# Performance work log

Measured on AMD Instinct MI355X. Metric: run time of the kernel, lower is better.

The kernel has to match this reference:

```python
import jax, jax.numpy as jnp
import numpy as np

N_HEADS = 16
N_KV_HEADS = 4
HEAD_DIM = 128


def _rope(x, cos, sin):
    # x: [b, s, h, d]; cos/sin: [s, d//2]; interleaved pair rotation
    b, s, h, d = x.shape
    xp = x.reshape(b, s, h, d // 2, 2)
    x_r, x_i = xp[..., 0], xp[..., 1]
    c = cos[None, :, None, :]
    sn = sin[None, :, None, :]
    o_r = x_r * c - x_i * sn
    o_i = x_r * sn + x_i * c
    return jnp.stack([o_r, o_i], axis=-1).reshape(b, s, h, d)


def setup_inputs() -> dict:
    key = jax.random.key(0)
    ks = jax.random.split(key, 7)
    B, S, D = 2, 2048, 2048
    KV = N_KV_HEADS * HEAD_DIM
    x = jax.random.normal(ks[0], (B, S, D), dtype=jnp.float32)
    freqs_cos = jax.random.uniform(ks[1], (S, HEAD_DIM // 2), dtype=jnp.float32)
    freqs_sin = jax.random.uniform(ks[2], (S, HEAD_DIM // 2), dtype=jnp.float32)
    scale = 0.02
    wq = jax.random.normal(ks[3], (D, D), dtype=jnp.float32) * scale
    wk = jax.random.normal(ks[4], (KV, D), dtype=jnp.float32) * scale
    wv = jax.random.normal(ks[5], (KV, D), dtype=jnp.float32) * scale
    wo = jax.random.normal(ks[6], (D, D), dtype=jnp.float32) * scale
    return {"x": x, "freqs_cos": freqs_cos, "freqs_sin": freqs_sin,
            "wq": wq, "wk": wk, "wv": wv, "wo": wo}


def reference(x, freqs_cos, freqs_sin, wq, wk, wv, wo):
    B, S, D = x.shape
    n_rep = N_HEADS // N_KV_HEADS
    q = (x @ wq.T).reshape(B, S, N_HEADS, HEAD_DIM)
    k = (x @ wk.T).reshape(B, S, N_KV_HEADS, HEAD_DIM)
    v = (x @ wv.T).reshape(B, S, N_KV_HEADS, HEAD_DIM)
    q = _rope(q, freqs_cos, freqs_sin)
    k = _rope(k, freqs_cos, freqs_sin)
    # repeat_kv == torch.repeat_interleave along head dim
    k = jnp.repeat(k, n_rep, axis=2)
    v = jnp.repeat(v, n_rep, axis=2)
    q = q.transpose(0, 2, 1, 3)  # [B, H, S, d]
    k = k.transpose(0, 2, 1, 3)
    v = v.transpose(0, 2, 1, 3)
    scale = 1.0 / np.sqrt(HEAD_DIM).astype(np.float32)
    scores = jnp.einsum('bhqd,bhkd->bhqk', q, k) * scale
    causal = jnp.tril(jnp.ones((S, S), dtype=bool))
    scores = jnp.where(causal[None, None], scores, jnp.finfo(jnp.float32).min)
    probs = jax.nn.softmax(scores.astype(jnp.float32), axis=-1).astype(q.dtype)
    out = jnp.einsum('bhqk,bhkd->bhqd', probs, v)
    out = out.transpose(0, 2, 1, 3).reshape(B, S, N_HEADS * HEAD_DIM)
    return out @ wo.T
```

## Files before the change

### kernel.cpp

```cpp
#include <hip/hip_runtime.h>
#include <hip/hip_bf16.h>
#include <type_traits>

using bf16x8 = __attribute__((ext_vector_type(8))) short;
using f32x4  = __attribute__((ext_vector_type(4))) float;
using u16x8  = __attribute__((ext_vector_type(8))) unsigned short;
using u16x4  = __attribute__((ext_vector_type(4))) unsigned short;
using u32x4  = __attribute__((ext_vector_type(4))) unsigned int;

__device__ __forceinline__ float b2f(unsigned short u) {
    unsigned int x = ((unsigned int)u) << 16;
    return __builtin_bit_cast(float, x);
}
__device__ __forceinline__ unsigned short f2b(float f) {
    __hip_bfloat16 h = __float2bfloat16(f);
    return __builtin_bit_cast(unsigned short, h);
}

#if defined(__has_builtin)
#if __has_builtin(__builtin_amdgcn_exp2f)
#define EXP2F(x) __builtin_amdgcn_exp2f(x)
#else
#define EXP2F(x) exp2f(x)
#endif
#else
#define EXP2F(x) exp2f(x)
#endif

__device__ __forceinline__ void async_copy16(const void* g, void* l) {
    __builtin_amdgcn_global_load_lds(
        (const __attribute__((address_space(1))) unsigned int*)g,
        (__attribute__((address_space(3))) unsigned int*)l, 16, 0, 0);
}

#define MFMA16(a, b, c) __builtin_amdgcn_mfma_f32_16x16x32_bf16(a, b, c, 0, 0, 0)

#define BARRIER() do { asm volatile("" ::: "memory"); \
    __builtin_amdgcn_s_barrier(); asm volatile("" ::: "memory"); } while (0)
#define VMCNT6() asm volatile("s_waitcnt vmcnt(6)" ::: "memory")
#define VMCNT0() asm volatile("s_waitcnt vmcnt(0)" ::: "memory")

__global__ __launch_bounds__(256) void cvt_f32_to_bf16(
    const float* __restrict__ s, unsigned short* __restrict__ d, int n4)
{
    int i = blockIdx.x * blockDim.x + threadIdx.x;
    if (i >= n4) return;
    float4 v = ((const float4*)s)[i];
    ushort4 o;
    o.x = f2b(v.x); o.y = f2b(v.y); o.z = f2b(v.z); o.w = f2b(v.w);
    ((ushort4*)d)[i] = o;
}

__global__ __launch_bounds__(512, 2) void qkv_gemm(
    const unsigned short* __restrict__ A,
    const unsigned short* __restrict__ Wq,
    const unsigned short* __restrict__ Wk,
    const unsigned short* __restrict__ Wv,
    unsigned short* __restrict__ Q,
    unsigned short* __restrict__ Kk,
    unsigned short* __restrict__ V)
{
    const int K = 2048;
    __shared__ unsigned short ldsA[2][256 * 64];
    __shared__ unsigned short ldsB[2][256 * 64];

    int tid  = threadIdx.x;
    int w    = tid >> 6;
    int lane = tid & 63;
    int idx  = lane & 15;
    int quad = lane >> 4;
    int srow   = lane >> 3;
    int schunk = (lane & 7) ^ srow;

    int wfm = (w >> 2) * 64;
    int wfn = (w & 3) * 64;

    int bid = (blockIdx.x & 7) * 24 + (blockIdx.x >> 3);
    int bm = bid / 12;
    int bn = bid - bm * 12;
    int m0 = bm * 256;

    const unsigned short* Bt;
    unsigned short* C;
    int Nc, n0;
    if (bn < 8)       { Bt = Wq + (size_t)bn * 256 * K;        C = Q;  Nc = 2048; n0 = bn * 256; }
    else if (bn < 10) { Bt = Wk + (size_t)(bn - 8) * 256 * K;  C = Kk; Nc = 512;  n0 = (bn - 8) * 256; }
    else              { Bt = Wv + (size_t)(bn - 10) * 256 * K; C = V;  Nc = 512;  n0 = (bn - 10) * 256; }

    const unsigned short* Ab = A + (size_t)m0 * K;

    f32x4 acc[8][4];
    #pragma unroll
    for (int mf = 0; mf < 8; ++mf)
        #pragma unroll
        for (int nf = 0; nf < 4; ++nf) acc[mf][nf] = (f32x4){0.f, 0.f, 0.f, 0.f};

    bf16x8 a[4][2], b0[2][2], b1[2][2];

    auto STAGE = [&](const unsigned short* __restrict__ G, int rb, int kc,
                     unsigned short* dst) {
        #pragma unroll
        for (int i = 0; i < 2; ++i) {
            int R = (w * 2 + i) * 8;
            async_copy16(G + (size_t)(rb + R + srow) * K + kc + schunk * 8,
                         dst + (size_t)R * 64);
        }
    };
    auto LDA = [&](int d, int mh) {
        #pragma unroll
        for (int mi = 0; mi < 4; ++mi) {
            int r = mh * 128 + wfm + mi * 16 + idx;
            #pragma unroll
            for (int ks = 0; ks < 2; ++ks)
                a[mi][ks] = *(const bf16x8*)&ldsA[d][r * 64 + (((ks * 4 + quad) ^ (r & 7)) << 3)];
        }
    };
    auto LDB0 = [&](int d, int nh) {
        #pragma unroll
        for (int nj = 0; nj < 2; ++nj) {
            int r = wfn + nh * 32 + nj * 16 + idx;
            #pragma unroll
            for (int ks = 0; ks < 2; ++ks)
                b0[nj][ks] = *(const bf16x8*)&ldsB[d][r * 64 + (((ks * 4 + quad) ^ (r & 7)) << 3)];
        }
    };
    auto LDB1 = [&](int d, int nh) {
        #pragma unroll
        for (int nj = 0; nj < 2; ++nj) {
            int r = wfn + nh * 32 + nj * 16 + idx;
            #pragma unroll
            for (int ks = 0; ks < 2; ++ks)
                b1[nj][ks] = *(const bf16x8*)&ldsB[d][r * 64 + (((ks * 4 + quad) ^ (r & 7)) << 3)];
        }
    };
    auto MM0 = [&](int mh, int nh) {
        __builtin_amdgcn_s_setprio(1);
        #pragma unroll
        for (int mi = 0; mi < 4; ++mi)
            #pragma unroll
            for (int nj = 0; nj < 2; ++nj)
                #pragma unroll
                for (int ks = 0; ks < 2; ++ks)
                    acc[mh * 4 + mi][nh * 2 + nj] =
                        MFMA16(a[mi][ks], b0[nj][ks], acc[mh * 4 + mi][nh * 2 + nj]);
        __builtin_amdgcn_s_setprio(0);
    };
    auto MM1 = [&](int mh, int nh) {
        __builtin_amdgcn_s_setprio(1);
        #pragma unroll
        for (int mi = 0; mi < 4; ++mi)
            #pragma unroll
            for (int nj = 0; nj < 2; ++nj)
                #pragma unroll
                for (int ks = 0; ks < 2; ++ks)
                    acc[mh * 4 + mi][nh * 2 + nj] =
                        MFMA16(a[mi][ks], b1[nj][ks], acc[mh * 4 + mi][nh * 2 + nj]);
        __builtin_amdgcn_s_setprio(0);
    };

    STAGE(Ab, 0,   0,  &ldsA[0][0]);
    STAGE(Ab, 128, 0,  &ldsA[0][128 * 64]);
    STAGE(Bt, 0,   0,  &ldsB[0][0]);
    STAGE(Bt, 128, 0,  &ldsB[0][128 * 64]);
    STAGE(Ab, 0,   64, &ldsA[1][0]);
    STAGE(Bt, 0,   64, &ldsB[1][0]);
    STAGE(Bt, 128, 64, &ldsB[1][128 * 64]);
    VMCNT6();
    BARRIER();

    for (int it = 0; it < 15; ++it) {
        int u = 2 * it;
        LDA(0, 0); LDB0(0, 0);
        STAGE(Ab, 128, (u + 1) * 64, &ldsA[1][128 * 64]);
        BARRIER(); MM0(0, 0); BARRIER();
        LDB1(0, 1);
        STAGE(Ab, 0, (u + 2) * 64, &ldsA[0][0]);
        BARRIER(); MM1(0, 1); BARRIER();
        LDA(0, 1);
        STAGE(Bt, 0, (u + 2) * 64, &ldsB[0][0]);
        BARRIER(); MM1(1, 1); BARRIER();
        STAGE(Bt, 128, (u + 2) * 64, &ldsB[0][128 * 64]);
        VMCNT6();
        BARRIER(); MM0(1, 0); BARRIER();
        LDA(1, 0); LDB0(1, 0);
        STAGE(Ab, 128, (u + 2) * 64, &ldsA[0][128 * 64]);
        BARRIER(); MM0(0, 0); BARRIER();
        LDB1(1, 1);
        STAGE(Ab, 0, (u + 3) * 64, &ldsA[1][0]);
        BARRIER(); MM1(0, 1); BARRIER();
        LDA(1, 1);
        STAGE(Bt, 0, (u + 3) * 64, &ldsB[1][0]);
        BARRIER(); MM1(1, 1); BARRIER();
        STAGE(Bt, 128, (u + 3) * 64, &ldsB[1][128 * 64]);
        VMCNT6();
        BARRIER(); MM0(1, 0); BARRIER();
    }

    LDA(0, 0); LDB0(0, 0);
    STAGE(Ab, 128, 31 * 64, &ldsA[1][128 * 64]);
    BARRIER(); MM0(0, 0); BARRIER();
    LDB1(0, 1);
    BARRIER(); MM1(0, 1); BARRIER();
    LDA(0, 1);
    BARRIER(); MM1(1, 1); BARRIER();
    VMCNT0();
    BARRIER(); MM0(1, 0); BARRIER();
    LDA(1, 0); LDB0(1, 0);
    BARRIER(); MM0(0, 0); BARRIER();
    LDB1(1, 1);
    BARRIER(); MM1(0, 1); BARRIER();
    LDA(1, 1);
    BARRIER(); MM1(1, 1); BARRIER();
    MM0(1, 0);

    #pragma unroll
    for (int mf = 0; mf < 8; ++mf) {
        #pragma unroll
        for (int r = 0; r < 4; ++r) {
            size_t row = (size_t)(m0 + (mf >> 2) * 128 + wfm + (mf & 3) * 16 + quad * 4 + r);
            #pragma unroll
            for (int nf = 0; nf < 4; ++nf) {
                int col = n0 + wfn + nf * 16 + idx;
                C[row * Nc + col] = f2b(acc[mf][nf][r]);
            }
        }
    }
}

__device__ __forceinline__ void g_stage(
    const unsigned short* __restrict__ A, const unsigned short* __restrict__ Bt,
    unsigned short* As, unsigned short* Bs,
    int k0, int K, int w, int srow, int schunk)
{
    #pragma unroll
    for (int i = 0; i < 4; ++i) {
        int cb = w * 4 + i;
        size_t goff = (size_t)(cb * 8 + srow) * K + k0 + schunk * 8;
        async_copy16(A  + goff, &As[cb * 512]);
        async_copy16(Bt + goff, &Bs[cb * 512]);
    }
}
__device__ __forceinline__ void g_compute(
    const unsigned short* As, const unsigned short* Bs,
    f32x4 (&acc)[4][4], int wm, int wn, int idx, int quad)
{
    #pragma unroll
    for (int ks = 0; ks < 2; ++ks) {
        bf16x8 af[4], bfr[4];
        #pragma unroll
        for (int mi = 0; mi < 4; ++mi) {
            int row = wm + mi * 16 + idx;
            af[mi] = *(const bf16x8*)&As[row * 64 + (((ks * 4 + quad) ^ (row & 7)) * 8)];
        }
        #pragma unroll
        for (int ni = 0; ni < 4; ++ni) {
            int row = wn + ni * 16 + idx;
            bfr[ni] = *(const bf16x8*)&Bs[row * 64 + (((ks * 4 + quad) ^ (row & 7)) * 8)];
        }
        #pragma unroll
        for (int mi = 0; mi < 4; ++mi)
            #pragma unroll
            for (int ni = 0; ni < 4; ++ni)
                acc[mi][ni] = MFMA16(af[mi], bfr[ni], acc[mi][ni]);
    }
}

template <typename OutT>
__global__ __launch_bounds__(256) void gemm_tile(
    const unsigned short* __restrict__ A,
    const unsigned short* __restrict__ Bt,
    OutT* __restrict__ C,
    int M, int N, int K)
{
    constexpr int BK = 64;
    __shared__ unsigned short As0[128 * BK];
    __shared__ unsigned short Bs0[128 * BK];
    __shared__ unsigned short As1[128 * BK];
    __shared__ unsigned short Bs1[128 * BK];

    int tid  = threadIdx.x;
    int w    = tid >> 6;
    int lane = tid & 63;
    int idx  = lane & 15;
    int quad = lane >> 4;
    int wm   = (w >> 1) * 64;
    int wn   = (w & 1) * 64;

    int tilesN = N / 128;
    int bm = blockIdx.x / tilesN;
    int bn = blockIdx.x - bm * tilesN;
    int m0 = bm * 128, n0 = bn * 128;

    const unsigned short* Ab = A  + (size_t)m0 * K;
    const unsigned short* Bb = Bt + (size_t)n0 * K;

    int srow   = lane >> 3;
    int schunk = (lane & 7) ^ srow;

    f32x4 acc[4][4];
    #pragma unroll
    for (int mi = 0; mi < 4; ++mi)
        #pragma unroll
        for (int ni = 0; ni < 4; ++ni) acc[mi][ni] = (f32x4){0.f, 0.f, 0.f, 0.f};

    g_stage(Ab, Bb, As0, Bs0, 0, K, w, srow, schunk);
    __syncthreads();

    for (int k0 = 0; k0 < K; k0 += 2 * BK) {
        if (k0 + BK < K)
            g_stage(Ab, Bb, As1, Bs1, k0 + BK, K, w, srow, schunk);
        g_compute(As0, Bs0, acc, wm, wn, idx, quad);
        __syncthreads();
        if (k0 + 2 * BK < K)
            g_stage(Ab, Bb, As0, Bs0, k0 + 2 * BK, K, w, srow, schunk);
        g_compute(As1, Bs1, acc, wm, wn, idx, quad);
        __syncthreads();
    }

    #pragma unroll
    for (int mi = 0; mi < 4; ++mi) {
        #pragma unroll
        for (int r = 0; r < 4; ++r) {
            size_t row = (size_t)(m0 + wm + mi * 16 + quad * 4 + r);
            #pragma unroll
            for (int ni = 0; ni < 4; ++ni) {
                int col = n0 + wn + ni * 16 + idx;
                if constexpr (std::is_same_v<OutT, float>) {
                    C[row * N + col] = acc[mi][ni][r];
                } else {
                    C[row * N + col] = f2b(acc[mi][ni][r]);
                }
            }
        }
    }
}

__global__ __launch_bounds__(256) void rope_kernel(
    unsigned short* __restrict__ x,
    const float* __restrict__ cs,
    const float* __restrict__ sn,
    int H, int total, float oscale)
{
    int e = blockIdx.x * blockDim.x + threadIdx.x;
    if (e >= total) return;
    int i = e & 63;
    int s = (e / (64 * H)) & 2047;
    float xr = b2f(x[2 * e]);
    float xi = b2f(x[2 * e + 1]);
    float c  = cs[s * 64 + i];
    float sv = sn[s * 64 + i];
    x[2 * e]     = f2b((xr * c - xi * sv) * oscale);
    x[2 * e + 1] = f2b((xr * sv + xi * c) * oscale);
}

__global__ __launch_bounds__(512, 4) void flash_attn(
    const unsigned short* __restrict__ qg,
    const unsigned short* __restrict__ kk,
    const unsigned short* __restrict__ vv,
    unsigned short* __restrict__ out)
{
    const int S = 2048;
    int bid = blockIdx.x;
    int qp  = bid & 15;
    int bh  = bid >> 4;
    int h   = bh & 15;
    int b   = bh >> 4;
    int kvh = h >> 2;

    int p   = b ? (15 - qp) : qp;

    int tid  = threadIdx.x;
    int w    = tid >> 6;
    int lane = tid & 63;
    int idx  = lane & 15;
    int quad = lane >> 4;

    int qt  = 2 * p + (w >> 2);
    int q0  = qt * 64;
    int wq0 = q0 + (w & 3) * 16;
    int qr  = wq0 + idx;

    __shared__ unsigned short Ks[32 * 128];
    __shared__ unsigned short Vt[128 * 40];

    const unsigned short* kbase = kk + ((size_t)b * S * 4 + kvh) * 128;
    const unsigned short* vbase = vv + ((size_t)b * S * 4 + kvh) * 128;

    bf16x8 qf[4];
    {
        const unsigned short* qpp =
            qg + ((size_t)((b * S + wq0 + idx) * 16 + h)) * 128 + quad * 8;
        #pragma unroll
        for (int ko = 0; ko < 4; ++ko)
            qf[ko] = *(const bf16x8*)(qpp + ko * 32);
    }

    f32x4 acc[8];
    #pragma unroll
    for (int n = 0; n < 8; ++n) acc[n] = (f32x4){0.f, 0.f, 0.f, 0.f};
    float lsum = 0.f;

    int dp = (tid & 63) * 2;
    int jb = (tid >> 6) & 3;
    int ih = (tid >> 8) * 4;

    int vcol = (((jb ^ ((dp >> 3) & 3)) << 3) + ih);

    int nt = 4 * p + 4;

    for (int t = 0; t < nt; ++t) {
        {
            int key = w * 4 + (lane >> 4);
            int sc  = (lane & 15) ^ (key & 7);
            async_copy16(kbase + ((size_t)(t * 32 + key)) * 512 + sc * 8,
                         &Ks[w * 512]);
        }
        {
            const unsigned short* vc = vbase + ((size_t)(t * 32 + jb * 4)) * 512 + dp;
            unsigned int ld[4];
            #pragma unroll
            for (int i = 0; i < 4; ++i) {
                int ii  = ih + i;
                int key = (ii >> 1) + 16 * (ii & 1);
                ld[i] = *(const unsigned int*)(vc + key * 512);
            }
            u16x4 lo, hi;
            #pragma unroll
            for (int i = 0; i < 4; ++i) {
                lo[i] = (unsigned short)ld[i];
                hi[i] = (unsigned short)(ld[i] >> 16);
            }
            *(u16x4*)&Vt[dp * 40 + vcol]       = lo;
            *(u16x4*)&Vt[(dp + 1) * 40 + vcol] = hi;
        }
        __syncthreads();

        if (t * 32 <= wq0 + 15) {
            f32x4 s0 = {0.f,0.f,0.f,0.f}, s1 = {0.f,0.f,0.f,0.f};
            #pragma unroll
            for (int ko = 0; ko < 4; ++ko) {
                int kc = ko * 4 + quad;
                bf16x8 kf0 = *(const bf16x8*)&Ks[idx * 128 + ((kc ^ (idx & 7)) * 8)];
                bf16x8 kf1 = *(const bf16x8*)&Ks[(16 + idx) * 128 + ((kc ^ (idx & 7)) * 8)];
                s0 = MFMA16(kf0, qf[ko], s0);
                s1 = MFMA16(kf1, qf[ko], s1);
            }
            unsigned int pk[4];
            if (t * 32 + 31 <= wq0) {
                #pragma unroll
                for (int r = 0; r < 4; ++r) {
                    float p0 = EXP2F(s0[r]);
                    float p1 = EXP2F(s1[r]);
                    lsum += p0 + p1;
                    pk[r] = (unsigned int)f2b(p0) | ((unsigned int)f2b(p1) << 16);
                }
            } else {
                int L = qr - t * 32;
                #pragma unroll
                for (int r = 0; r < 4; ++r) {
                    int kl = quad * 4 + r;
                    float p0 = (kl      <= L) ? EXP2F(s0[r]) : 0.f;
                    float p1 = (kl + 16 <= L) ? EXP2F(s1[r]) : 0.f;
                    lsum += p0 + p1;
                    pk[r] = (unsigned int)f2b(p0) | ((unsigned int)f2b(p1) << 16);
                }
            }
            u32x4 pku = {pk[0], pk[1], pk[2], pk[3]};
            bf16x8 pf = __builtin_bit_cast(bf16x8, pku);
            #pragma unroll
            for (int n = 0; n < 8; ++n) {
                int rr = n * 16 + idx;
                bf16x8 vf = *(const bf16x8*)&Vt[rr * 40 + ((quad ^ ((rr >> 3) & 3)) << 3)];
                acc[n] = MFMA16(vf, pf, acc[n]);
            }
        }
        __syncthreads();
    }

    lsum += __shfl_xor(lsum, 16);
    lsum += __shfl_xor(lsum, 32);
    float inv = 1.f / lsum;
    size_t rowb = (size_t)(b * S + wq0 + idx) * 2048 + h * 128;
    #pragma unroll
    for (int n = 0; n < 8; ++n) {
        ushort4 o;
        o.x = f2b(acc[n][0] * inv);
        o.y = f2b(acc[n][1] * inv);
        o.z = f2b(acc[n][2] * inv);
        o.w = f2b(acc[n][3] * inv);
        *(ushort4*)&out[rowb + n * 16 + quad * 4] = o;
    }
}

extern "C" void kernel_launch(void* const* d_in, const int* in_sizes, int n_in,
                              void* d_out, int out_size, void* d_ws, size_t ws_size,
                              hipStream_t stream)
{
    const float* x  = (const float*)d_in[0];
    const float* fc = (const float*)d_in[1];
    const float* fs = (const float*)d_in[2];
    const float* wq = (const float*)d_in[3];
    const float* wk = (const float*)d_in[4];
    const float* wv = (const float*)d_in[5];
    const float* wo = (const float*)d_in[6];
    float* out = (float*)d_out;

    const int B = 2, S = 2048, D = 2048, KV = 512;
    const int M = B * S;

    unsigned short* ws  = (unsigned short*)d_ws;
    unsigned short* xb  = ws;
    unsigned short* wqb = xb  + (size_t)M * D;
    unsigned short* wkb = wqb + (size_t)D * D;
    unsigned short* wvb = wkb + (size_t)KV * D;
    unsigned short* wob = wvb + (size_t)KV * D;
    unsigned short* qb  = wob + (size_t)D * D;
    unsigned short* kb  = qb  + (size_t)M * D;
    unsigned short* vb  = kb  + (size_t)M * KV;
    unsigned short* ao  = vb  + (size_t)M * KV;

    cvt_f32_to_bf16<<<dim3((M * D / 4) / 256), dim3(256), 0, stream>>>(x,  xb,  M * D / 4);
    cvt_f32_to_bf16<<<dim3((D * D / 4) / 256), dim3(256), 0, stream>>>(wq, wqb, D * D / 4);
    cvt_f32_to_bf16<<<dim3((KV * D / 4) / 256), dim3(256), 0, stream>>>(wk, wkb, KV * D / 4);
    cvt_f32_to_bf16<<<dim3((KV * D / 4) / 256), dim3(256), 0, stream>>>(wv, wvb, KV * D / 4);
    cvt_f32_to_bf16<<<dim3((D * D / 4) / 256), dim3(256), 0, stream>>>(wo, wob, D * D / 4);

    qkv_gemm<<<dim3(192), dim3(512), 0, stream>>>(xb, wqb, wkb, wvb, qb, kb, vb);

    int qpairs = B * S * 16 * 64;
    int kpairs = B * S * 4 * 64;
    const float c2 = 0.12752584f;
    rope_kernel<<<dim3(qpairs / 256), dim3(256), 0, stream>>>(qb, fc, fs, 16, qpairs, c2);
    rope_kernel<<<dim3(kpairs / 256), dim3(256), 0, stream>>>(kb, fc, fs, 4, kpairs, 1.0f);

    flash_attn<<<dim3(512), dim3(512), 0, stream>>>(qb, kb, vb, ao);

    gemm_tile<float><<<dim3((M / 128) * (D / 128)), dim3(256), 0, stream>>>(ao, wob, out, M, D, D);
}
```

Baseline: 326.7 us.

## Double-buffer K/V tiles in attention loop and rework V transpose via lane shuffles

The attention kernel now keeps two LDS buffers for K and transposed V, and issues the global loads for tile t+1 before computing on tile t. The loaded V data is written to LDS only after compute, so load latency overlaps the MFMA work and the first barrier per iteration goes away. The V transpose is also rewritten so each thread writes one 16-byte row using a lane-pair shuffle, replacing two 8-byte stores. This doubles LDS use and raises register pressure, which may lower occupancy.

```diff
diff --git a/kernel.cpp b/kernel.cpp
--- a/kernel.cpp
+++ b/kernel.cpp
@@ -380,8 +380,8 @@
     int wq0 = q0 + (w & 3) * 16;
     int qr  = wq0 + idx;
 
-    __shared__ unsigned short Ks[32 * 128];
-    __shared__ unsigned short Vt[128 * 40];
+    __shared__ unsigned short Ks[2][32 * 128];
+    __shared__ unsigned short Vt[2][128 * 40];
 
     const unsigned short* kbase = kk + ((size_t)b * S * 4 + kvh) * 128;
     const unsigned short* vbase = vv + ((size_t)b * S * 4 + kvh) * 128;
@@ -400,48 +400,61 @@
     for (int n = 0; n < 8; ++n) acc[n] = (f32x4){0.f, 0.f, 0.f, 0.f};
     float lsum = 0.f;
 
-    int dp = (tid & 63) * 2;
-    int jb = (tid >> 6) & 3;
-    int ih = (tid >> 8) * 4;
-
-    int vcol = (((jb ^ ((dp >> 3) & 3)) << 3) + ih);
+    int s_   = w & 3;
+    int vr   = (w >> 2) * 64 + lane;
+    int vodd = lane & 1;
+    int cpb  = vr & ~1;
+    int vwoff = vr * 40 + ((s_ ^ ((vr >> 3) & 3)) << 3);
+
+    int key = w * 4 + (lane >> 4);
+    int ksc = (lane & 15) ^ (key & 7);
 
     int nt = 4 * p + 4;
 
+    unsigned int vld[4];
+
+    auto STAGE_ISSUE = [&](int t, int d) {
+        async_copy16(kbase + ((size_t)(t * 32 + key)) * 512 + ksc * 8,
+                     &Ks[d][w * 512]);
+        const unsigned short* vc = vbase + ((size_t)t * 32) * 512 + cpb;
+        #pragma unroll
+        for (int i = 0; i < 4; ++i) {
+            int ii = vodd * 4 + i;
+            int gk = s_ * 4 + (ii >> 1) + 16 * (ii & 1);
+            vld[i] = *(const unsigned int*)(vc + (size_t)gk * 512);
+        }
+    };
+    auto STAGE_WRITE = [&](int d) {
+        unsigned int L01 = (vld[0] & 0xffffu) | (vld[1] << 16);
+        unsigned int L23 = (vld[2] & 0xffffu) | (vld[3] << 16);
+        unsigned int H01 = (vld[0] >> 16) | (vld[1] & 0xffff0000u);
+        unsigned int H23 = (vld[2] >> 16) | (vld[3] & 0xffff0000u);
+        unsigned int x0 = vodd ? L01 : H01;
+        unsigned int x1 = vodd ? L23 : H23;
+        unsigned int y0 = __shfl_xor(x0, 1);
+        unsigned int y1 = __shfl_xor(x1, 1);
+        u32x4 row;
+        if (vodd) row = (u32x4){y0, y1, H01, H23};
+        else      row = (u32x4){L01, L23, y0, y1};
+        *(u32x4*)&Vt[d][vwoff] = row;
+    };
+
+    STAGE_ISSUE(0, 0);
+    VMCNT0();
+    STAGE_WRITE(0);
+    __syncthreads();
+
     for (int t = 0; t < nt; ++t) {
-        {
-            int key = w * 4 + (lane >> 4);
-            int sc  = (lane & 15) ^ (key & 7);
-            async_copy16(kbase + ((size_t)(t * 32 + key)) * 512 + sc * 8,
-                         &Ks[w * 512]);
-        }
-        {
-            const unsigned short* vc = vbase + ((size_t)(t * 32 + jb * 4)) * 512 + dp;
-            unsigned int ld[4];
-            #pragma unroll
-            for (int i = 0; i < 4; ++i) {
-                int ii  = ih + i;
-                int key = (ii >> 1) + 16 * (ii & 1);
-                ld[i] = *(const unsigned int*)(vc + key * 512);
-            }
-            u16x4 lo, hi;
-            #pragma unroll
-            for (int i = 0; i < 4; ++i) {
-                lo[i] = (unsigned short)ld[i];
-                hi[i] = (unsigned short)(ld[i] >> 16);
-            }
-            *(u16x4*)&Vt[dp * 40 + vcol]       = lo;
-            *(u16x4*)&Vt[(dp + 1) * 40 + vcol] = hi;
-        }
-        __syncthreads();
+        int bc = t & 1;
+        if (t + 1 < nt) STAGE_ISSUE(t + 1, bc ^ 1);
 
         if (t * 32 <= wq0 + 15) {
             f32x4 s0 = {0.f,0.f,0.f,0.f}, s1 = {0.f,0.f,0.f,0.f};
             #pragma unroll
             for (int ko = 0; ko < 4; ++ko) {
                 int kc = ko * 4 + quad;
-                bf16x8 kf0 = *(const bf16x8*)&Ks[idx * 128 + ((kc ^ (idx & 7)) * 8)];
-                bf16x8 kf1 = *(const bf16x8*)&Ks[(16 + idx) * 128 + ((kc ^ (idx & 7)) * 8)];
+                bf16x8 kf0 = *(const bf16x8*)&Ks[bc][idx * 128 + ((kc ^ (idx & 7)) * 8)];
+                bf16x8 kf1 = *(const bf16x8*)&Ks[bc][(16 + idx) * 128 + ((kc ^ (idx & 7)) * 8)];
                 s0 = MFMA16(kf0, qf[ko], s0);
                 s1 = MFMA16(kf1, qf[ko], s1);
             }
@@ -470,9 +483,14 @@
             #pragma unroll
             for (int n = 0; n < 8; ++n) {
                 int rr = n * 16 + idx;
-                bf16x8 vf = *(const bf16x8*)&Vt[rr * 40 + ((quad ^ ((rr >> 3) & 3)) << 3)];
+                bf16x8 vf = *(const bf16x8*)&Vt[bc][rr * 40 + ((quad ^ ((rr >> 3) & 3)) << 3)];
                 acc[n] = MFMA16(vf, pf, acc[n]);
             }
+        }
+
+        if (t + 1 < nt) {
+            VMCNT0();
+            STAGE_WRITE(bc ^ 1);
         }
         __syncthreads();
     }
```

Measured after the change: 317.6 us. 2.8% less time.
